# Kernel optimization log

Measured on AMD Instinct MI355X. Metric: run time of the kernel, lower is better.

## Reference

```python
import jax, jax.numpy as jnp
import numpy as np

L = 5        # n_layers
H = 8        # heads
DH = 32      # dim_head = n_hidden // heads
D = 256      # n_hidden
KR = 4       # key_ratio
QKD = KR * DH  # 128, q/k feature dim
IN = 3       # fun_dim + space_dim
OUT = 1      # out_dim
N = 32768    # number of mesh points
EPS = 1e-5

def _ln(x, g, b):
    m = jnp.mean(x, axis=-1, keepdims=True)
    v = jnp.var(x, axis=-1, keepdims=True)
    return (x - m) * jax.lax.rsqrt(v + EPS) * g + b

def _gelu(x):
    return jax.nn.gelu(x, approximate=False)  # torch nn.GELU default (erf)

def setup_inputs() -> dict:
    key = jax.random.key(0)
    ks = iter(jax.random.split(key, 64))
    def w(*s):
        return jax.random.normal(next(ks), s, jnp.float32) * 0.02
    return {
        "x": jax.random.normal(next(ks), (N, IN), jnp.float32),
        # preprocess MLP: Linear(IN,2D)+GELU, Linear(2D,D)
        "pre_w1": w(IN, 2 * D), "pre_b1": jnp.zeros((2 * D,), jnp.float32),
        "pre_w2": w(2 * D, D), "pre_b2": jnp.zeros((D,), jnp.float32),
        "placeholder": jax.random.uniform(next(ks), (D,), jnp.float32) / D,
        # per-block params stacked over L
        "ln1_g": jnp.ones((L, D), jnp.float32), "ln1_b": jnp.zeros((L, D), jnp.float32),
        "inp_w": w(L, D, D), "inp_b": jnp.zeros((L, D), jnp.float32),
        "temp_q": jnp.full((L, H), 0.5, jnp.float32), "temp_k": jnp.full((L, H), 0.5, jnp.float32),
        "wq": w(L, DH, QKD), "wk": w(L, DH, QKD), "wv": w(L, DH, DH),
        "out_w1": w(L, D, D), "out_b1": jnp.zeros((L, D), jnp.float32),
        "out_w2": w(L, D, D), "out_b2": jnp.zeros((L, D), jnp.float32),
        "ln2_g": jnp.ones((L, D), jnp.float32), "ln2_b": jnp.zeros((L, D), jnp.float32),
        "mlp_w1": w(L, D, D), "mlp_b1": jnp.zeros((L, D), jnp.float32),  # mlp_ratio=1 -> hidden=D
        "mlp_w2": w(L, D, D), "mlp_b2": jnp.zeros((L, D), jnp.float32),
        # last-layer head
        "ln3_g": jnp.ones((D,), jnp.float32), "ln3_b": jnp.zeros((D,), jnp.float32),
        "head_w": w(D, OUT), "head_b": jnp.zeros((OUT,), jnp.float32),
    }

def reference(x, pre_w1, pre_b1, pre_w2, pre_b2, placeholder,
              ln1_g, ln1_b, inp_w, inp_b, temp_q, temp_k, wq, wk, wv,
              out_w1, out_b1, out_w2, out_b2, ln2_g, ln2_b,
              mlp_w1, mlp_b1, mlp_w2, mlp_b2, ln3_g, ln3_b, head_w, head_b):
    # preprocess + placeholder bias
    fx = _gelu(x[None] @ pre_w1 + pre_b1) @ pre_w2 + pre_b2  # [1, N, D]
    fx = fx + placeholder
    for i in range(L):
        # --- LinearNO attention block ---
        h = _ln(fx, ln1_g[i], ln1_b[i])
        xm = h @ inp_w[i] + inp_b[i]                       # [1, N, D]
        xm = xm.reshape(1, N, H, DH).transpose(0, 2, 1, 3)  # [1, H, N, DH]
        q = jnp.einsum('bhnd,de->bhne', xm, wq[i])          # [1, H, N, QKD]
        k = jnp.einsum('bhnd,de->bhne', xm, wk[i])          # [1, H, N, QKD]
        v = jnp.einsum('bhnd,dc->bhnc', xm, wv[i])          # [1, H, N, DH]
        tq = jnp.clip(temp_q[i], 0.1, 2.0)[None, :, None, None]
        tk = jnp.clip(temp_k[i], 0.1, 2.0)[None, :, None, None]
        q = jax.nn.softmax(q / tq, axis=-1)  # over feature dim
        k = jax.nn.softmax(k / tk, axis=-2)  # over point dim
        kv = jnp.einsum('bhnd,bhnc->bhdc', k, v)    # [1, H, QKD, DH]
        qkv = jnp.einsum('bhnd,bhdc->bhnc', q, kv)  # [1, H, N, DH]
        qkv = qkv.transpose(0, 2, 1, 3).reshape(1, N, D)
        attn = _gelu(qkv @ out_w1[i] + out_b1[i]) @ out_w2[i] + out_b2[i]
        fx = attn + fx
        # --- MLP block (n_layers=0, res=False: pre + post only) ---
        h2 = _ln(fx, ln2_g[i], ln2_b[i])
        fx = _gelu(h2 @ mlp_w1[i] + mlp_b1[i]) @ mlp_w2[i] + mlp_b2[i] + fx
    # last block head: mlp2(ln_3(fx))
    out = _ln(fx, ln3_g, ln3_b) @ head_w + head_b  # [1, N, OUT]
    return out[0]  # module returns fx[0]
```

## Files before the change

### kernel.cpp

```cpp
#include <hip/hip_runtime.h>
#include <hip/hip_bf16.h>
#include <math.h>

constexpr int NP  = 32768;
constexpr int HH  = 8;

typedef short bf16x8 __attribute__((ext_vector_type(8)));
typedef float f32x4  __attribute__((ext_vector_type(4)));

__device__ __forceinline__ float gelu_f(float x) {
    return 0.5f * x * (1.0f + erff(x * 0.70710678118654752f));
}

__device__ __forceinline__ unsigned short f2bf(float x) {
    union { float f; unsigned u; } v; v.f = x;
    unsigned r = v.u + 0x7fffu + ((v.u >> 16) & 1u);
    return (unsigned short)(r >> 16);
}

__device__ __forceinline__ float bf2f(unsigned short h) {
    union { unsigned u; float f; } v; v.u = ((unsigned)h) << 16;
    return v.f;
}

__global__ __launch_bounds__(256) void transpose_bf16_k(
    const float* __restrict__ src, unsigned short* __restrict__ dst, int K)
{
    __shared__ float tile[32][33];
    int g = blockIdx.z;
    int k0 = blockIdx.x * 32, c0 = blockIdx.y * 32;
    int tx = threadIdx.x & 31, ty = threadIdx.x >> 5;
    const float* s = src + (size_t)g * K * 256;
    unsigned short* d = dst + (size_t)g * 256 * K;
    #pragma unroll
    for (int rr = 0; rr < 4; ++rr) {
        int r = ty + rr * 8;
        tile[r][tx] = s[(size_t)(k0 + r) * 256 + c0 + tx];
    }
    __syncthreads();
    #pragma unroll
    for (int rr = 0; rr < 4; ++rr) {
        int r = ty + rr * 8;
        d[(size_t)(c0 + r) * K + k0 + tx] = f2bf(tile[tx][r]);
    }
}

__global__ __launch_bounds__(256) void transpose_scale_bf16_k(
    const float* __restrict__ src, const float* __restrict__ g,
    unsigned short* __restrict__ dst, int K)
{
    __shared__ float tile[32][33];
    int z = blockIdx.z;
    int k0 = blockIdx.x * 32, c0 = blockIdx.y * 32;
    int tx = threadIdx.x & 31, ty = threadIdx.x >> 5;
    const float* s = src + (size_t)z * K * 256;
    unsigned short* d = dst + (size_t)z * 256 * K;
    #pragma unroll
    for (int rr = 0; rr < 4; ++rr) {
        int r = ty + rr * 8;
        tile[r][tx] = s[(size_t)(k0 + r) * 256 + c0 + tx];
    }
    __syncthreads();
    float gs = g[z * 256 + k0 + tx];
    #pragma unroll
    for (int rr = 0; rr < 4; ++rr) {
        int r = ty + rr * 8;
        d[(size_t)(c0 + r) * K + k0 + tx] = f2bf(gs * tile[tx][r]);
    }
}

__global__ __launch_bounds__(256) void colsum_k(
    const float* __restrict__ W, const float* __restrict__ g,
    const float* __restrict__ b, float* __restrict__ c2, float* __restrict__ c1)
{
    int z = blockIdx.z, c = threadIdx.x;
    const float* Wz = W + (size_t)z * 65536;
    const float* gz = g + z * 256;
    const float* bz = b + z * 256;
    float s2 = 0.f, s1 = 0.f;
    for (int k = 0; k < 256; ++k) {
        float w = Wz[k * 256 + c];
        s2 += gz[k] * w;
        s1 += bz[k] * w;
    }
    c2[z * 256 + c] = s2;
    c1[z * 256 + c] = s1;
}

__global__ __launch_bounds__(256) void prep_wkvT(
    const float* __restrict__ wk, const float* __restrict__ wv,
    const float* __restrict__ wq,
    unsigned short* __restrict__ wkT, unsigned short* __restrict__ wvT,
    unsigned short* __restrict__ wqT)
{
    int l = blockIdx.x, tid = threadIdx.x;
    for (int idx = tid; idx < 4096; idx += 256) {
        int d = idx >> 5, k = idx & 31;
        wkT[l * 4096 + idx] = f2bf(wk[l * 4096 + k * 128 + d]);
        wqT[l * 4096 + idx] = f2bf(wq[l * 4096 + k * 128 + d]);
    }
    for (int idx = tid; idx < 1024; idx += 256) {
        int c = idx >> 5, k = idx & 31;
        wvT[l * 1024 + idx] = f2bf(wv[l * 1024 + k * 32 + c]);
    }
}

template<bool GENA, bool AF32, bool LNFOLD, bool DOGELU, bool RESID, bool STATS, bool PERM>
__global__ __launch_bounds__(256) void gemm_bf(
    const unsigned short* __restrict__ Ah, const float* __restrict__ Af,
    const unsigned short* __restrict__ Wt,
    const float* __restrict__ bias, const float* __restrict__ bias2,
    float* __restrict__ outF, unsigned short* __restrict__ outH,
    const float* __restrict__ stats_in, float* __restrict__ stats_out,
    const float* __restrict__ c1v, const float* __restrict__ c2vec,
    const float* __restrict__ genx, const float* __restrict__ genw1,
    const float* __restrict__ genb1, int K)
{
    __shared__ __align__(16) unsigned short As[128 * 64];
    __shared__ __align__(16) unsigned short Bs[128 * 64];
    __shared__ float rmean[LNFOLD ? 128 : 1];
    __shared__ float rrstd[LNFOLD ? 128 : 1];
    __shared__ float w1s[GENA ? 1536 : 1];
    __shared__ float b1s[GENA ? 512 : 1];
    __shared__ float x3s[GENA ? 512 : 1];

    const int tid = threadIdx.x;
    const int rBase = blockIdx.x * 128, cBase = blockIdx.y * 128;

    if constexpr (GENA) {
        for (int i2 = tid; i2 < 1536; i2 += 256) w1s[i2] = genw1[i2];
        for (int i2 = tid; i2 < 512; i2 += 256) b1s[i2] = genb1[i2];
        if (tid < 128) {
            x3s[tid * 4 + 0] = genx[(size_t)(rBase + tid) * 3 + 0];
            x3s[tid * 4 + 1] = genx[(size_t)(rBase + tid) * 3 + 1];
            x3s[tid * 4 + 2] = genx[(size_t)(rBase + tid) * 3 + 2];
        }
        __syncthreads();
    }
    if constexpr (LNFOLD) {
        if (tid < 128) {
            const float* sp = stats_in + (size_t)(rBase + tid) * 8;
            float4 s0 = *(const float4*)sp;
            float4 s1 = *(const float4*)(sp + 4);
            float mean = (s0.x + s0.z + s1.x + s1.z) * (1.f / 256.f);
            float ex2  = (s0.y + s0.w + s1.y + s1.w) * (1.f / 256.f);
            rmean[tid] = mean;
            rrstd[tid] = rsqrtf(fmaxf(ex2 - mean * mean, 0.f) + 1e-5f);
        }
        __syncthreads();
    }

    f32x4 acc[4][4];
    #pragma unroll
    for (int i = 0; i < 4; ++i)
        #pragma unroll
        for (int j = 0; j < 4; ++j)
            acc[i][j] = (f32x4){0.f, 0.f, 0.f, 0.f};

    const int lane = tid & 63, wid = tid >> 6;
    const int wr = wid >> 1, wc = wid & 1;
    const int lrow = lane & 15, quad = lane >> 4;
    const int srow = tid >> 3;
    const int sch  = tid & 7;

    for (int kc = 0; kc < K; kc += 64) {
        if constexpr (GENA) {
            #pragma unroll
            for (int it = 0; it < 4; ++it) {
                int row = srow + it * 32;
                float x0 = x3s[row * 4 + 0], x1 = x3s[row * 4 + 1], x2 = x3s[row * 4 + 2];
                unsigned short pk[8];
                #pragma unroll
                for (int j = 0; j < 8; ++j) {
                    int k = kc + sch * 8 + j;
                    float t = x0 * w1s[k] + x1 * w1s[512 + k] + x2 * w1s[1024 + k] + b1s[k];
                    pk[j] = f2bf(gelu_f(t));
                }
                *(uint4*)&As[row * 64 + ((sch ^ (row & 7)) << 3)] = *(uint4*)pk;
            }
        } else if constexpr (AF32) {
            #pragma unroll
            for (int it = 0; it < 4; ++it) {
                int row = srow + it * 32;
                const float* ap = Af + (size_t)(rBase + row) * K + kc + sch * 8;
                float4 a0 = *(const float4*)ap;
                float4 a1 = *(const float4*)(ap + 4);
                unsigned short pk[8];
                pk[0] = f2bf(a0.x); pk[1] = f2bf(a0.y); pk[2] = f2bf(a0.z); pk[3] = f2bf(a0.w);
                pk[4] = f2bf(a1.x); pk[5] = f2bf(a1.y); pk[6] = f2bf(a1.z); pk[7] = f2bf(a1.w);
                *(uint4*)&As[row * 64 + ((sch ^ (row & 7)) << 3)] = *(uint4*)pk;
            }
        } else {
            #pragma unroll
            for (int it = 0; it < 4; ++it) {
                int row = srow + it * 32;
                uint4 av = *(const uint4*)(Ah + (size_t)(rBase + row) * K + kc + sch * 8);
                *(uint4*)&As[row * 64 + ((sch ^ (row & 7)) << 3)] = av;
            }
        }
        #pragma unroll
        for (int it = 0; it < 4; ++it) {
            int n = srow + it * 32;
            uint4 wv_ = *(const uint4*)(Wt + (size_t)(cBase + n) * K + kc + sch * 8);
            *(uint4*)&Bs[n * 64 + ((sch ^ (n & 7)) << 3)] = wv_;
        }
        __syncthreads();
        #pragma unroll
        for (int ks = 0; ks < 2; ++ks) {
            bf16x8 af[4], bfr[4];
            #pragma unroll
            for (int t = 0; t < 4; ++t) {
                int row = wr * 64 + t * 16 + lrow;
                af[t] = *(bf16x8*)&As[row * 64 + (((ks * 4 + quad) ^ (row & 7)) << 3)];
                int n = wc * 64 + t * 16 + lrow;
                bfr[t] = *(bf16x8*)&Bs[n * 64 + (((ks * 4 + quad) ^ (n & 7)) << 3)];
            }
            #pragma unroll
            for (int ti = 0; ti < 4; ++ti)
                #pragma unroll
                for (int tj = 0; tj < 4; ++tj)
                    acc[ti][tj] = __builtin_amdgcn_mfma_f32_16x16x32_bf16(
                        af[ti], bfr[tj], acc[ti][tj], 0, 0, 0);
        }
        __syncthreads();
    }

    float c1b[4], c2r[4];
    #pragma unroll
    for (int tj = 0; tj < 4; ++tj) {
        int gcol = cBase + wc * 64 + tj * 16 + lrow;
        float b = bias[gcol];
        if (bias2) b += bias2[gcol];
        if constexpr (LNFOLD) {
            c1b[tj] = c1v[gcol] + b;
            c2r[tj] = c2vec[gcol];
        } else {
            c1b[tj] = b;
            c2r[tj] = 0.f;
        }
    }
    #pragma unroll
    for (int ti = 0; ti < 4; ++ti) {
        #pragma unroll
        for (int r = 0; r < 4; ++r) {
            int rib = wr * 64 + ti * 16 + quad * 4 + r;
            int grow = rBase + rib;
            float mean = 0.f, rstd = 1.f;
            if constexpr (LNFOLD) { mean = rmean[rib]; rstd = rrstd[rib]; }
            float vv[4];
            #pragma unroll
            for (int tj = 0; tj < 4; ++tj) {
                float t = acc[ti][tj][r];
                float v;
                if constexpr (LNFOLD) v = rstd * (t - mean * c2r[tj]) + c1b[tj];
                else                  v = t + c1b[tj];
                if constexpr (DOGELU) v = gelu_f(v);
                vv[tj] = v;
            }
            if constexpr (RESID) {
                #pragma unroll
                for (int tj = 0; tj < 4; ++tj) {
                    int gcol = cBase + wc * 64 + tj * 16 + lrow;
                    vv[tj] += outF[(size_t)grow * 256 + gcol];
                }
            }
            if constexpr (STATS) {
                float rs = vv[0] + vv[1] + vv[2] + vv[3];
                float rq = vv[0]*vv[0] + vv[1]*vv[1] + vv[2]*vv[2] + vv[3]*vv[3];
                #pragma unroll
                for (int m = 1; m < 16; m <<= 1) {
                    rs += __shfl_xor(rs, m);
                    rq += __shfl_xor(rq, m);
                }
                if (lrow == 0) {
                    stats_out[(size_t)grow * 8 + (blockIdx.y * 2 + wc) * 2 + 0] = rs;
                    stats_out[(size_t)grow * 8 + (blockIdx.y * 2 + wc) * 2 + 1] = rq;
                }
            }
            #pragma unroll
            for (int tj = 0; tj < 4; ++tj) {
                int gcol = cBase + wc * 64 + tj * 16 + lrow;
                if constexpr (PERM) {
                    size_t pidx = (size_t)(gcol >> 5) * NP * 32 + (size_t)grow * 32 + (gcol & 31);
                    if (outF) outF[pidx] = vv[tj];
                    if (outH) outH[pidx] = f2bf(vv[tj]);
                } else {
                    if (outF) outF[(size_t)grow * 256 + gcol] = vv[tj];
                    if (outH) outH[(size_t)grow * 256 + gcol] = f2bf(vv[tj]);
                }
            }
        }
    }
}

template<bool AF32, bool LNFOLD>
__global__ __launch_bounds__(256) void gemm_lgl(
    const unsigned short* __restrict__ Ah, const float* __restrict__ Af,
    const unsigned short* __restrict__ W1t, const unsigned short* __restrict__ W2t,
    const float* __restrict__ b1, const float* __restrict__ b2,
    float* __restrict__ fx,
    const float* __restrict__ stats_in, float* __restrict__ stats_out,
    const float* __restrict__ c1v, const float* __restrict__ c2vec)
{
    __shared__ __align__(16) unsigned short As[64 * 64];
    __shared__ __align__(16) unsigned short Bs[256 * 64];
    __shared__ __align__(16) unsigned short Ts[64 * 256];
    __shared__ float rmean[LNFOLD ? 64 : 1];
    __shared__ float rrstd[LNFOLD ? 64 : 1];

    const int tid = threadIdx.x;
    const int rBase = blockIdx.x * 64;
    const int lane = tid & 63, wid = tid >> 6;
    const int lrow = lane & 15, quad = lane >> 4;

    if constexpr (LNFOLD) {
        if (tid < 64) {
            const float* sp = stats_in + (size_t)(rBase + tid) * 8;
            float4 s0 = *(const float4*)sp;
            float4 s1 = *(const float4*)(sp + 4);
            float mean = (s0.x + s0.z + s1.x + s1.z) * (1.f / 256.f);
            float ex2  = (s0.y + s0.w + s1.y + s1.w) * (1.f / 256.f);
            rmean[tid] = mean;
            rrstd[tid] = rsqrtf(fmaxf(ex2 - mean * mean, 0.f) + 1e-5f);
        }
    }

    f32x4 acc[4][4];
    #pragma unroll
    for (int i = 0; i < 4; ++i)
        #pragma unroll
        for (int j = 0; j < 4; ++j)
            acc[i][j] = (f32x4){0.f, 0.f, 0.f, 0.f};

    for (int kc = 0; kc < 256; kc += 64) {
        #pragma unroll
        for (int it = 0; it < 2; ++it) {
            int idx = tid + it * 256;
            int row = idx >> 3, sch = idx & 7;
            if constexpr (AF32) {
                const float* ap = Af + (size_t)(rBase + row) * 256 + kc + sch * 8;
                float4 a0 = *(const float4*)ap;
                float4 a1 = *(const float4*)(ap + 4);
                unsigned short pk[8];
                pk[0] = f2bf(a0.x); pk[1] = f2bf(a0.y); pk[2] = f2bf(a0.z); pk[3] = f2bf(a0.w);
                pk[4] = f2bf(a1.x); pk[5] = f2bf(a1.y); pk[6] = f2bf(a1.z); pk[7] = f2bf(a1.w);
                *(uint4*)&As[row * 64 + ((sch ^ (row & 7)) << 3)] = *(uint4*)pk;
            } else {
                uint4 av = *(const uint4*)(Ah + (size_t)(rBase + row) * 256 + kc + sch * 8);
                *(uint4*)&As[row * 64 + ((sch ^ (row & 7)) << 3)] = av;
            }
        }
        #pragma unroll
        for (int it = 0; it < 8; ++it) {
            int idx = tid + it * 256;
            int n = idx >> 3, sch = idx & 7;
            uint4 wv_ = *(const uint4*)(W1t + (size_t)n * 256 + kc + sch * 8);
            *(uint4*)&Bs[n * 64 + ((sch ^ (n & 7)) << 3)] = wv_;
        }
        __syncthreads();
        #pragma unroll
        for (int ks = 0; ks < 2; ++ks) {
            bf16x8 af[4], bfr[4];
            #pragma unroll
            for (int t = 0; t < 4; ++t) {
                int row = t * 16 + lrow;
                af[t] = *(bf16x8*)&As[row * 64 + (((ks * 4 + quad) ^ (row & 7)) << 3)];
                int n = wid * 64 + t * 16 + lrow;
                bfr[t] = *(bf16x8*)&Bs[n * 64 + (((ks * 4 + quad) ^ (n & 7)) << 3)];
            }
            #pragma unroll
            for (int ti = 0; ti < 4; ++ti)
                #pragma unroll
                for (int tj = 0; tj < 4; ++tj)
                    acc[ti][tj] = __builtin_amdgcn_mfma_f32_16x16x32_bf16(
                        af[ti], bfr[tj], acc[ti][tj], 0, 0, 0);
        }
        __syncthreads();
    }

    {
        float c1b[4], c2r[4];
        #pragma unroll
        for (int tj = 0; tj < 4; ++tj) {
            int gcol = wid * 64 + tj * 16 + lrow;
            if constexpr (LNFOLD) {
                c1b[tj] = c1v[gcol] + b1[gcol];
                c2r[tj] = c2vec[gcol];
            } else {
                c1b[tj] = b1[gcol];
                c2r[tj] = 0.f;
            }
        }
        #pragma unroll
        for (int ti = 0; ti < 4; ++ti) {
            #pragma unroll
            for (int r = 0; r < 4; ++r) {
                int row = ti * 16 + quad * 4 + r;
                float mean = 0.f, rstd = 1.f;
                if constexpr (LNFOLD) { mean = rmean[row]; rstd = rrstd[row]; }
                #pragma unroll
                for (int tj = 0; tj < 4; ++tj) {
                    float t = acc[ti][tj][r];
                    float v;
                    if constexpr (LNFOLD) v = rstd * (t - mean * c2r[tj]) + c1b[tj];
                    else                  v = t + c1b[tj];
                    v = gelu_f(v);
                    int col = wid * 64 + tj * 16 + lrow;
                    int ch = col >> 3;
                    Ts[row * 256 + ((ch ^ (row & 7)) << 3) + (col & 7)] = f2bf(v);
                }
            }
        }
    }
    __syncthreads();

    f32x4 acc2[4][4];
    #pragma unroll
    for (int i = 0; i < 4; ++i)
        #pragma unroll
        for (int j = 0; j < 4; ++j)
            acc2[i][j] = (f32x4){0.f, 0.f, 0.f, 0.f};

    for (int kc = 0; kc < 256; kc += 64) {
        #pragma unroll
        for (int it = 0; it < 8; ++it) {
            int idx = tid + it * 256;
            int n = idx >> 3, sch = idx & 7;
            uint4 wv_ = *(const uint4*)(W2t + (size_t)n * 256 + kc + sch * 8);
            *(uint4*)&Bs[n * 64 + ((sch ^ (n & 7)) << 3)] = wv_;
        }
        __syncthreads();
        #pragma unroll
        for (int ks = 0; ks < 2; ++ks) {
            bf16x8 af[4], bfr[4];
            #pragma unroll
            for (int t = 0; t < 4; ++t) {
                int row = t * 16 + lrow;
                int ch = (kc >> 3) + ks * 4 + quad;
                af[t] = *(bf16x8*)&Ts[row * 256 + ((ch ^ (row & 7)) << 3)];
                int n = wid * 64 + t * 16 + lrow;
                bfr[t] = *(bf16x8*)&Bs[n * 64 + (((ks * 4 + quad) ^ (n & 7)) << 3)];
            }
            #pragma unroll
            for (int ti = 0; ti < 4; ++ti)
                #pragma unroll
                for (int tj = 0; tj < 4; ++tj)
                    acc2[ti][tj] = __builtin_amdgcn_mfma_f32_16x16x32_bf16(
                        af[ti], bfr[tj], acc2[ti][tj], 0, 0, 0);
        }
        __syncthreads();
    }

    float bb[4];
    #pragma unroll
    for (int tj = 0; tj < 4; ++tj) bb[tj] = b2[wid * 64 + tj * 16 + lrow];
    #pragma unroll
    for (int ti = 0; ti < 4; ++ti) {
        #pragma unroll
        for (int r = 0; r < 4; ++r) {
            int grow = rBase + ti * 16 + quad * 4 + r;
            float vv[4];
            #pragma unroll
            for (int tj = 0; tj < 4; ++tj) {
                int gcol = wid * 64 + tj * 16 + lrow;
                vv[tj] = acc2[ti][tj][r] + bb[tj] + fx[(size_t)grow * 256 + gcol];
            }
            float rs = vv[0] + vv[1] + vv[2] + vv[3];
            float rq = vv[0]*vv[0] + vv[1]*vv[1] + vv[2]*vv[2] + vv[3]*vv[3];
            #pragma unroll
            for (int m = 1; m < 16; m <<= 1) {
                rs += __shfl_xor(rs, m);
                rq += __shfl_xor(rq, m);
            }
            if (lrow == 0) {
                stats_out[(size_t)grow * 8 + wid * 2 + 0] = rs;
                stats_out[(size_t)grow * 8 + wid * 2 + 1] = rq;
            }
            #pragma unroll
            for (int tj = 0; tj < 4; ++tj) {
                int gcol = wid * 64 + tj * 16 + lrow;
                fx[(size_t)grow * 256 + gcol] = vv[tj];
            }
        }
    }
}

__global__ __launch_bounds__(256) void kv6_kernel(
    const unsigned short* __restrict__ xm2h, const unsigned short* __restrict__ wkT,
    const unsigned short* __restrict__ wvT, const float* __restrict__ tk_arr,
    float* __restrict__ partials, int layer)
{
    __shared__ __align__(16) unsigned short xs[64 * 32];
    __shared__ __align__(16) unsigned short wks[128 * 32];
    __shared__ __align__(16) unsigned short wvs[32 * 32];
    __shared__ __align__(16) unsigned short els[128 * 72];
    __shared__ __align__(16) unsigned short vls[32 * 72];
    __shared__ float sums[4 * 128];

    const int tid = threadIdx.x;
    const int h = blockIdx.y;
    const int rowBase = blockIdx.x * 512;
    const int w = tid >> 6, lane = tid & 63;
    const int lrow = lane & 15, quad = lane >> 4;

    float tk = fminf(fmaxf(tk_arr[layer * 8 + h], 0.1f), 2.0f);
    float invtk = 1.0f / tk;

    #pragma unroll
    for (int it = 0; it < 2; ++it) {
        int cid = tid + it * 256;
        int d = cid >> 2, kc = cid & 3;
        uint4 v = *(const uint4*)(wkT + d * 32 + kc * 8);
        *(uint4*)&wks[d * 32 + ((kc ^ (d & 3)) << 3)] = v;
    }
    if (tid < 128) {
        int c = tid >> 2, kc = tid & 3;
        uint4 v = *(const uint4*)(wvT + c * 32 + kc * 8);
        *(uint4*)&wvs[c * 32 + ((kc ^ (c & 3)) << 3)] = v;
    }

    f32x4 acc2[2][2];
    #pragma unroll
    for (int di = 0; di < 2; ++di)
        #pragma unroll
        for (int ci = 0; ci < 2; ++ci)
            acc2[di][ci] = (f32x4){0.f, 0.f, 0.f, 0.f};
    float seacc[8];
    #pragma unroll
    for (int dt = 0; dt < 8; ++dt) seacc[dt] = 0.f;

    const unsigned short* src = xm2h + (size_t)h * NP * 32 + (size_t)rowBase * 32;

    for (int sub = 0; sub < 8; ++sub) {
        __syncthreads();
        {
            int row = tid >> 2, kc = tid & 3;
            uint4 v = *(const uint4*)(src + (size_t)(sub * 64 + row) * 32 + kc * 8);
            *(uint4*)&xs[row * 32 + ((kc ^ (row & 3)) << 3)] = v;
        }
        __syncthreads();
        int arow = w * 16 + lrow;
        bf16x8 ax = *(bf16x8*)&xs[arow * 32 + ((quad ^ (arow & 3)) << 3)];
        #pragma unroll
        for (int ct = 0; ct < 2; ++ct) {
            int c = ct * 16 + lrow;
            bf16x8 bw = *(bf16x8*)&wvs[c * 32 + ((quad ^ (c & 3)) << 3)];
            f32x4 cc = (f32x4){0.f, 0.f, 0.f, 0.f};
            cc = __builtin_amdgcn_mfma_f32_16x16x32_bf16(ax, bw, cc, 0, 0, 0);
            unsigned short pk[4];
            pk[0] = f2bf(cc[0]); pk[1] = f2bf(cc[1]);
            pk[2] = f2bf(cc[2]); pk[3] = f2bf(cc[3]);
            *(uint2*)&vls[(ct * 16 + lrow) * 72 + w * 16 + quad * 4] = *(uint2*)pk;
        }
        #pragma unroll
        for (int dt = 0; dt < 8; ++dt) {
            int d = dt * 16 + lrow;
            bf16x8 bw = *(bf16x8*)&wks[d * 32 + ((quad ^ (d & 3)) << 3)];
            f32x4 cc = (f32x4){0.f, 0.f, 0.f, 0.f};
            cc = __builtin_amdgcn_mfma_f32_16x16x32_bf16(ax, bw, cc, 0, 0, 0);
            unsigned short pk[4];
            float se = 0.f;
            #pragma unroll
            for (int r = 0; r < 4; ++r) {
                float l = fminf(fmaxf(cc[r] * invtk, -30.f), 30.f);
                unsigned short eb = f2bf(__expf(l));
                pk[r] = eb;
                se += bf2f(eb);
            }
            seacc[dt] += se;
            *(uint2*)&els[d * 72 + w * 16 + quad * 4] = *(uint2*)pk;
        }
        __syncthreads();
        #pragma unroll
        for (int di = 0; di < 2; ++di) {
            int dm = (2 * w + di) * 16 + lrow;
            #pragma unroll
            for (int ks = 0; ks < 2; ++ks) {
                bf16x8 ae = *(bf16x8*)&els[dm * 72 + ks * 32 + quad * 8];
                #pragma unroll
                for (int ci = 0; ci < 2; ++ci) {
                    int cn = ci * 16 + lrow;
                    bf16x8 bv = *(bf16x8*)&vls[cn * 72 + ks * 32 + quad * 8];
                    acc2[di][ci] = __builtin_amdgcn_mfma_f32_16x16x32_bf16(
                        ae, bv, acc2[di][ci], 0, 0, 0);
                }
            }
        }
    }

    float* outp = partials + ((size_t)h * 64 + blockIdx.x) * 4224;
    #pragma unroll
    for (int di = 0; di < 2; ++di)
        #pragma unroll
        for (int ci = 0; ci < 2; ++ci)
            #pragma unroll
            for (int r = 0; r < 4; ++r) {
                int d = (2 * w + di) * 16 + quad * 4 + r;
                int c = ci * 16 + lrow;
                outp[d * 32 + c] = acc2[di][ci][r];
            }
    #pragma unroll
    for (int dt = 0; dt < 8; ++dt) {
        float s = seacc[dt];
        s += __shfl_xor(s, 16);
        s += __shfl_xor(s, 32);
        if (quad == 0) sums[w * 128 + dt * 16 + lrow] = s;
    }
    __syncthreads();
    if (tid < 128)
        outp[4096 + tid] = sums[tid] + sums[128 + tid] + sums[256 + tid] + sums[384 + tid];
}

__global__ __launch_bounds__(256) void kv_reduce_kernel(
    const float* __restrict__ partials, unsigned short* __restrict__ kvT,
    float* __restrict__ sumexp)
{
    int gid = blockIdx.x * 256 + threadIdx.x;
    if (gid >= 8 * 4224) return;
    int h = gid / 4224, idx = gid % 4224;
    const float* base = partials + (size_t)h * 64 * 4224 + idx;
    float s = 0.f;
    #pragma unroll 8
    for (int c = 0; c < 64; ++c) s += base[(size_t)c * 4224];
    if (idx < 4096) {
        int d = idx >> 5, c = idx & 31;
        kvT[(size_t)h * 4096 + c * 128 + d] = f2bf(s);
    } else {
        sumexp[h * 128 + (idx - 4096)] = s;
    }
}

__global__ __launch_bounds__(256) void qkv6_kernel(
    const unsigned short* __restrict__ xm2h, const unsigned short* __restrict__ wqT,
    const float* __restrict__ tq_arr, const unsigned short* __restrict__ kvT,
    const float* __restrict__ sumexp, unsigned short* __restrict__ outH, int layer)
{
    __shared__ __align__(16) unsigned short xs[64 * 32];
    __shared__ __align__(16) unsigned short wqs[128 * 32];
    __shared__ __align__(16) unsigned short kvb[32 * 136];
    __shared__ __align__(16) unsigned short els[64 * 136];
    __shared__ float ises[128];

    const int tid = threadIdx.x;
    const int h = blockIdx.y;
    const int rowBase = blockIdx.x * 64;
    const int w = tid >> 6, lane = tid & 63;
    const int lrow = lane & 15, quad = lane >> 4;

    float tq = fminf(fmaxf(tq_arr[layer * 8 + h], 0.1f), 2.0f);
    float invtq = 1.0f / tq;

    if (tid < 128) ises[tid] = 1.0f / sumexp[h * 128 + tid];
    #pragma unroll
    for (int it = 0; it < 2; ++it) {
        int cid = tid + it * 256;
        int d = cid >> 2, kc = cid & 3;
        uint4 v = *(const uint4*)(wqT + d * 32 + kc * 8);
        *(uint4*)&wqs[d * 32 + ((kc ^ (d & 3)) << 3)] = v;
    }
    #pragma unroll
    for (int it = 0; it < 2; ++it) {
        int cid = tid + it * 256;
        int c = cid >> 4, k8 = cid & 15;
        uint4 v = *(const uint4*)(kvT + (size_t)h * 4096 + c * 128 + k8 * 8);
        *(uint4*)&kvb[c * 136 + k8 * 8] = v;
    }
    {
        int row = tid >> 2, kc = tid & 3;
        uint4 v = *(const uint4*)(xm2h + (size_t)h * NP * 32 +
                                  (size_t)(rowBase + row) * 32 + kc * 8);
        *(uint4*)&xs[row * 32 + ((kc ^ (row & 3)) << 3)] = v;
    }
    __syncthreads();

    int arow = w * 16 + lrow;
    bf16x8 ax = *(bf16x8*)&xs[arow * 32 + ((quad ^ (arow & 3)) << 3)];
    f32x4 lg[8];
    #pragma unroll
    for (int dt = 0; dt < 8; ++dt) {
        int d = dt * 16 + lrow;
        bf16x8 bw = *(bf16x8*)&wqs[d * 32 + ((quad ^ (d & 3)) << 3)];
        f32x4 cc = (f32x4){0.f, 0.f, 0.f, 0.f};
        lg[dt] = __builtin_amdgcn_mfma_f32_16x16x32_bf16(ax, bw, cc, 0, 0, 0);
    }
    float isv[8];
    #pragma unroll
    for (int dt = 0; dt < 8; ++dt) isv[dt] = ises[dt * 16 + lrow];

    #pragma unroll
    for (int r = 0; r < 4; ++r) {
        float m = lg[0][r];
        #pragma unroll
        for (int dt = 1; dt < 8; ++dt) m = fmaxf(m, lg[dt][r]);
        m = fmaxf(m, __shfl_xor(m, 1));
        m = fmaxf(m, __shfl_xor(m, 2));
        m = fmaxf(m, __shfl_xor(m, 4));
        m = fmaxf(m, __shfl_xor(m, 8));
        float e[8], s = 0.f;
        #pragma unroll
        for (int dt = 0; dt < 8; ++dt) {
            e[dt] = __expf((lg[dt][r] - m) * invtq);
            s += e[dt];
        }
        s += __shfl_xor(s, 1);
        s += __shfl_xor(s, 2);
        s += __shfl_xor(s, 4);
        s += __shfl_xor(s, 8);
        float inv = 1.0f / s;
        int erow = w * 16 + quad * 4 + r;
        #pragma unroll
        for (int dt = 0; dt < 8; ++dt)
            els[erow * 136 + dt * 16 + lrow] = f2bf(e[dt] * inv * isv[dt]);
    }

    #pragma unroll
    for (int ct = 0; ct < 2; ++ct) {
        f32x4 oc = (f32x4){0.f, 0.f, 0.f, 0.f};
        #pragma unroll
        for (int ks = 0; ks < 4; ++ks) {
            bf16x8 ae = *(bf16x8*)&els[(w * 16 + lrow) * 136 + ks * 32 + quad * 8];
            bf16x8 bv = *(bf16x8*)&kvb[(ct * 16 + lrow) * 136 + ks * 32 + quad * 8];
            oc = __builtin_amdgcn_mfma_f32_16x16x32_bf16(ae, bv, oc, 0, 0, 0);
        }
        #pragma unroll
        for (int r = 0; r < 4; ++r)
            outH[(size_t)(rowBase + w * 16 + quad * 4 + r) * 256 +
                 h * 32 + ct * 16 + lrow] = f2bf(oc[r]);
    }
}

__global__ __launch_bounds__(256) void head_kernel(
    const float* __restrict__ fx, const float* __restrict__ g, const float* __restrict__ b,
    const float* __restrict__ hw, const float* __restrict__ hb, float* __restrict__ out)
{
    int lane = threadIdx.x & 63;
    int row = blockIdx.x * 4 + (threadIdx.x >> 6);
    float4 v = *(const float4*)(fx + (size_t)row * 256 + lane * 4);
    float s1 = v.x + v.y + v.z + v.w;
    float s2 = v.x * v.x + v.y * v.y + v.z * v.z + v.w * v.w;
    #pragma unroll
    for (int m = 1; m < 64; m <<= 1) { s1 += __shfl_xor(s1, m); s2 += __shfl_xor(s2, m); }
    float mean = s1 * 0.00390625f;
    float rstd = rsqrtf(fmaxf(s2 * 0.00390625f - mean * mean, 0.f) + 1e-5f);
    float4 gg = *(const float4*)(g + lane * 4);
    float4 bb = *(const float4*)(b + lane * 4);
    float4 w4 = *(const float4*)(hw + lane * 4);
    float d = ((v.x - mean) * rstd * gg.x + bb.x) * w4.x
            + ((v.y - mean) * rstd * gg.y + bb.y) * w4.y
            + ((v.z - mean) * rstd * gg.z + bb.z) * w4.z
            + ((v.w - mean) * rstd * gg.w + bb.w) * w4.w;
    #pragma unroll
    for (int m = 1; m < 64; m <<= 1) d += __shfl_xor(d, m);
    if (lane == 0) out[row] = d + hb[0];
}

extern "C" void kernel_launch(void* const* d_in, const int* in_sizes, int n_in,
                              void* d_out, int out_size, void* d_ws, size_t ws_size,
                              hipStream_t stream)
{
    const float* x      = (const float*)d_in[0];
    const float* pre_w1 = (const float*)d_in[1];
    const float* pre_b1 = (const float*)d_in[2];
    const float* pre_w2 = (const float*)d_in[3];
    const float* pre_b2 = (const float*)d_in[4];
    const float* ph     = (const float*)d_in[5];
    const float* ln1_g  = (const float*)d_in[6];
    const float* ln1_b  = (const float*)d_in[7];
    const float* inp_w  = (const float*)d_in[8];
    const float* inp_b  = (const float*)d_in[9];
    const float* temp_q = (const float*)d_in[10];
    const float* temp_k = (const float*)d_in[11];
    const float* wq     = (const float*)d_in[12];
    const float* wk     = (const float*)d_in[13];
    const float* wv     = (const float*)d_in[14];
    const float* out_w1 = (const float*)d_in[15];
    const float* out_b1 = (const float*)d_in[16];
    const float* out_w2 = (const float*)d_in[17];
    const float* out_b2 = (const float*)d_in[18];
    const float* ln2_g  = (const float*)d_in[19];
    const float* ln2_b  = (const float*)d_in[20];
    const float* mlp_w1 = (const float*)d_in[21];
    const float* mlp_b1 = (const float*)d_in[22];
    const float* mlp_w2 = (const float*)d_in[23];
    const float* mlp_b2 = (const float*)d_in[24];
    const float* ln3_g  = (const float*)d_in[25];
    const float* ln3_b  = (const float*)d_in[26];
    const float* head_w = (const float*)d_in[27];
    const float* head_b = (const float*)d_in[28];
    float* out = (float*)d_out;

    float* fx = (float*)d_ws;
    unsigned short* fxh = (unsigned short*)(fx + (size_t)NP * 256);
    unsigned short* ChH = fxh + (size_t)NP * 256;
    unsigned short* xm2h = ChH;
    float* scr = (float*)(ChH + (size_t)NP * 256);
    float* st = scr + (size_t)NP * 256;
    unsigned short* kvT = (unsigned short*)(st + (size_t)NP * 8);
    float* se = (float*)(kvT + 8 * 4096);
    float* c1i = se + 8 * 128;
    float* c2i = c1i + 1280;
    float* c1m = c2i + 1280;
    float* c2m = c1m + 1280;
    unsigned short* wtPre = (unsigned short*)(c2m + 1280);
    unsigned short* wtL   = wtPre + 256 * 512;
    unsigned short* wkT   = wtL + 25 * 65536;
    unsigned short* wvT   = wkT + 5 * 4096;
    unsigned short* wqT   = wvT + 5 * 1024;

    unsigned short* wtIn = wtL;
    unsigned short* wtO1 = wtL +  5 * 65536;
    unsigned short* wtO2 = wtL + 10 * 65536;
    unsigned short* wtM1 = wtL + 15 * 65536;
    unsigned short* wtM2 = wtL + 20 * 65536;

    unsigned short* qh = (unsigned short*)scr;

    dim3 bt(256);

    transpose_bf16_k<<<dim3(16, 8, 1), bt, 0, stream>>>(pre_w2, wtPre, 512);
    transpose_scale_bf16_k<<<dim3(8, 8, 5), bt, 0, stream>>>(inp_w,  ln1_g, wtIn, 256);
    transpose_bf16_k<<<dim3(8, 8, 5), bt, 0, stream>>>(out_w1, wtO1, 256);
    transpose_bf16_k<<<dim3(8, 8, 5), bt, 0, stream>>>(out_w2, wtO2, 256);
    transpose_scale_bf16_k<<<dim3(8, 8, 5), bt, 0, stream>>>(mlp_w1, ln2_g, wtM1, 256);
    transpose_bf16_k<<<dim3(8, 8, 5), bt, 0, stream>>>(mlp_w2, wtM2, 256);
    colsum_k<<<dim3(1, 1, 5), bt, 0, stream>>>(inp_w,  ln1_g, ln1_b, c2i, c1i);
    colsum_k<<<dim3(1, 1, 5), bt, 0, stream>>>(mlp_w1, ln2_g, ln2_b, c2m, c1m);
    prep_wkvT<<<dim3(5), bt, 0, stream>>>(wk, wv, wq, wkT, wvT, wqT);

    dim3 gg(256, 2);

    gemm_bf<true, false, false, false, false, true, false><<<gg, bt, 0, stream>>>(
        nullptr, nullptr, wtPre, pre_b2, ph, fx, nullptr, nullptr, st,
        nullptr, nullptr, x, pre_w1, pre_b1, 512);

    for (int i = 0; i < 5; ++i) {
        gemm_bf<false, true, true, false, false, false, true><<<gg, bt, 0, stream>>>(
            nullptr, fx, wtIn + (size_t)i * 65536, inp_b + i * 256, nullptr, nullptr, xm2h,
            st, nullptr, c1i + i * 256, c2i + i * 256, nullptr, nullptr, nullptr, 256);
        kv6_kernel<<<dim3(64, 8), bt, 0, stream>>>(
            xm2h, wkT + (size_t)i * 4096, wvT + (size_t)i * 1024, temp_k, scr, i);
        kv_reduce_kernel<<<dim3(132), bt, 0, stream>>>(scr, kvT, se);
        qkv6_kernel<<<dim3(512, 8), bt, 0, stream>>>(
            xm2h, wqT + (size_t)i * 4096, temp_q, kvT, se, qh, i);
        gemm_lgl<false, false><<<dim3(512), bt, 0, stream>>>(
            qh, nullptr, wtO1 + (size_t)i * 65536, wtO2 + (size_t)i * 65536,
            out_b1 + i * 256, out_b2 + i * 256, fx, nullptr, st, nullptr, nullptr);
        gemm_lgl<true, true><<<dim3(512), bt, 0, stream>>>(
            nullptr, fx, wtM1 + (size_t)i * 65536, wtM2 + (size_t)i * 65536,
            mlp_b1 + i * 256, mlp_b2 + i * 256, fx, st, st,
            c1m + i * 256, c2m + i * 256);
    }
    head_kernel<<<dim3(NP / 4), bt, 0, stream>>>(fx, ln3_g, ln3_b, head_w, head_b, out);
}
```

Before: 830.5 us.

## Fuse next layer's LN1+input projection into MLP gemm epilogue

The MLP gemm_lgl kernel now keeps its output rows in shared memory as bf16. It computes per-row LayerNorm statistics locally and runs the next layer's input-projection GEMM (LN folded via c1/c2 vectors) in the same kernel, writing xm2h directly. This removes one launch per layer and the re-read of fx and stats from global memory. The costs are extra register and LDS pressure in the fused kernel, and the last layer's stats are no longer written.

```diff
diff --git a/kernel.cpp b/kernel.cpp
--- a/kernel.cpp
+++ b/kernel.cpp
@@ -293,20 +293,25 @@
     }
 }
 
-template<bool AF32, bool LNFOLD>
+template<bool AF32, bool LNFOLD, bool WSTATS, bool NEXTW>
 __global__ __launch_bounds__(256) void gemm_lgl(
     const unsigned short* __restrict__ Ah, const float* __restrict__ Af,
     const unsigned short* __restrict__ W1t, const unsigned short* __restrict__ W2t,
     const float* __restrict__ b1, const float* __restrict__ b2,
     float* __restrict__ fx,
     const float* __restrict__ stats_in, float* __restrict__ stats_out,
-    const float* __restrict__ c1v, const float* __restrict__ c2vec)
+    const float* __restrict__ c1v, const float* __restrict__ c2vec,
+    const unsigned short* __restrict__ W3t, const float* __restrict__ b3,
+    const float* __restrict__ c1n, const float* __restrict__ c2n,
+    unsigned short* __restrict__ outNext)
 {
     __shared__ __align__(16) unsigned short As[64 * 64];
     __shared__ __align__(16) unsigned short Bs[256 * 64];
     __shared__ __align__(16) unsigned short Ts[64 * 256];
-    __shared__ float rmean[LNFOLD ? 64 : 1];
-    __shared__ float rrstd[LNFOLD ? 64 : 1];
+    __shared__ float rmean[(LNFOLD || NEXTW) ? 64 : 1];
+    __shared__ float rrstd[(LNFOLD || NEXTW) ? 64 : 1];
+    __shared__ float ssum[NEXTW ? 256 : 1];
+    __shared__ float ssq [NEXTW ? 256 : 1];
 
     const int tid = threadIdx.x;
     const int rBase = blockIdx.x * 64;
@@ -458,28 +463,118 @@
     for (int ti = 0; ti < 4; ++ti) {
         #pragma unroll
         for (int r = 0; r < 4; ++r) {
-            int grow = rBase + ti * 16 + quad * 4 + r;
+            int row = ti * 16 + quad * 4 + r;
+            int grow = rBase + row;
             float vv[4];
             #pragma unroll
             for (int tj = 0; tj < 4; ++tj) {
                 int gcol = wid * 64 + tj * 16 + lrow;
                 vv[tj] = acc2[ti][tj][r] + bb[tj] + fx[(size_t)grow * 256 + gcol];
             }
-            float rs = vv[0] + vv[1] + vv[2] + vv[3];
-            float rq = vv[0]*vv[0] + vv[1]*vv[1] + vv[2]*vv[2] + vv[3]*vv[3];
-            #pragma unroll
-            for (int m = 1; m < 16; m <<= 1) {
-                rs += __shfl_xor(rs, m);
-                rq += __shfl_xor(rq, m);
-            }
-            if (lrow == 0) {
-                stats_out[(size_t)grow * 8 + wid * 2 + 0] = rs;
-                stats_out[(size_t)grow * 8 + wid * 2 + 1] = rq;
+            if constexpr (WSTATS || NEXTW) {
+                float rs = vv[0] + vv[1] + vv[2] + vv[3];
+                float rq = vv[0]*vv[0] + vv[1]*vv[1] + vv[2]*vv[2] + vv[3]*vv[3];
+                #pragma unroll
+                for (int m = 1; m < 16; m <<= 1) {
+                    rs += __shfl_xor(rs, m);
+                    rq += __shfl_xor(rq, m);
+                }
+                if (lrow == 0) {
+                    if constexpr (WSTATS) {
+                        stats_out[(size_t)grow * 8 + wid * 2 + 0] = rs;
+                        stats_out[(size_t)grow * 8 + wid * 2 + 1] = rq;
+                    }
+                    if constexpr (NEXTW) {
+                        ssum[row * 4 + wid] = rs;
+                        ssq [row * 4 + wid] = rq;
+                    }
+                }
             }
             #pragma unroll
             for (int tj = 0; tj < 4; ++tj) {
                 int gcol = wid * 64 + tj * 16 + lrow;
                 fx[(size_t)grow * 256 + gcol] = vv[tj];
+                if constexpr (NEXTW) {
+                    int ch = gcol >> 3;
+                    Ts[row * 256 + ((ch ^ (row & 7)) << 3) + (gcol & 7)] = f2bf(vv[tj]);
+                }
+            }
+        }
+    }
+
+    if constexpr (NEXTW) {
+        __syncthreads();
+        if (tid < 64) {
+            float q0 = ssum[tid * 4 + 0], q1 = ssum[tid * 4 + 1];
+            float q2 = ssum[tid * 4 + 2], q3 = ssum[tid * 4 + 3];
+            float p0 = ssq [tid * 4 + 0], p1 = ssq [tid * 4 + 1];
+            float p2 = ssq [tid * 4 + 2], p3 = ssq [tid * 4 + 3];
+            float mean = (q0 + q1 + q2 + q3) * (1.f / 256.f);
+            float ex2  = (p0 + p1 + p2 + p3) * (1.f / 256.f);
+            rmean[tid] = mean;
+            rrstd[tid] = rsqrtf(fmaxf(ex2 - mean * mean, 0.f) + 1e-5f);
+        }
+        __syncthreads();
+
+        f32x4 acc3[4][4];
+        #pragma unroll
+        for (int i = 0; i < 4; ++i)
+            #pragma unroll
+            for (int j = 0; j < 4; ++j)
+                acc3[i][j] = (f32x4){0.f, 0.f, 0.f, 0.f};
+
+        for (int kc = 0; kc < 256; kc += 64) {
+            #pragma unroll
+            for (int it = 0; it < 8; ++it) {
+                int idx = tid + it * 256;
+                int n = idx >> 3, sch = idx & 7;
+                uint4 wv_ = *(const uint4*)(W3t + (size_t)n * 256 + kc + sch * 8);
+                *(uint4*)&Bs[n * 64 + ((sch ^ (n & 7)) << 3)] = wv_;
+            }
+            __syncthreads();
+            #pragma unroll
+            for (int ks = 0; ks < 2; ++ks) {
+                bf16x8 af[4], bfr[4];
+                #pragma unroll
+                for (int t = 0; t < 4; ++t) {
+                    int row = t * 16 + lrow;
+                    int ch = (kc >> 3) + ks * 4 + quad;
+                    af[t] = *(bf16x8*)&Ts[row * 256 + ((ch ^ (row & 7)) << 3)];
+                    int n = wid * 64 + t * 16 + lrow;
+                    bfr[t] = *(bf16x8*)&Bs[n * 64 + (((ks * 4 + quad) ^ (n & 7)) << 3)];
+                }
+                #pragma unroll
+                for (int ti = 0; ti < 4; ++ti)
+                    #pragma unroll
+                    for (int tj = 0; tj < 4; ++tj)
+                        acc3[ti][tj] = __builtin_amdgcn_mfma_f32_16x16x32_bf16(
+                            af[ti], bfr[tj], acc3[ti][tj], 0, 0, 0);
+            }
+            __syncthreads();
+        }
+
+        float c1b3[4], c2r3[4];
+        #pragma unroll
+        for (int tj = 0; tj < 4; ++tj) {
+            int gcol = wid * 64 + tj * 16 + lrow;
+            c1b3[tj] = c1n[gcol] + b3[gcol];
+            c2r3[tj] = c2n[gcol];
+        }
+        #pragma unroll
+        for (int ti = 0; ti < 4; ++ti) {
+            #pragma unroll
+            for (int r = 0; r < 4; ++r) {
+                int row = ti * 16 + quad * 4 + r;
+                int grow = rBase + row;
+                float mean = rmean[row], rstd = rrstd[row];
+                #pragma unroll
+                for (int tj = 0; tj < 4; ++tj) {
+                    int gcol = wid * 64 + tj * 16 + lrow;
+                    float t = acc3[ti][tj][r];
+                    float v = rstd * (t - mean * c2r3[tj]) + c1b3[tj];
+                    size_t pidx = (size_t)(gcol >> 5) * NP * 32 + (size_t)grow * 32 + (gcol & 31);
+                    outNext[pidx] = f2bf(v);
+                }
             }
         }
     }
@@ -833,22 +928,34 @@
         nullptr, nullptr, wtPre, pre_b2, ph, fx, nullptr, nullptr, st,
         nullptr, nullptr, x, pre_w1, pre_b1, 512);
 
+    gemm_bf<false, true, true, false, false, false, true><<<gg, bt, 0, stream>>>(
+        nullptr, fx, wtIn, inp_b, nullptr, nullptr, xm2h,
+        st, nullptr, c1i, c2i, nullptr, nullptr, nullptr, 256);
+
     for (int i = 0; i < 5; ++i) {
-        gemm_bf<false, true, true, false, false, false, true><<<gg, bt, 0, stream>>>(
-            nullptr, fx, wtIn + (size_t)i * 65536, inp_b + i * 256, nullptr, nullptr, xm2h,
-            st, nullptr, c1i + i * 256, c2i + i * 256, nullptr, nullptr, nullptr, 256);
         kv6_kernel<<<dim3(64, 8), bt, 0, stream>>>(
             xm2h, wkT + (size_t)i * 4096, wvT + (size_t)i * 1024, temp_k, scr, i);
         kv_reduce_kernel<<<dim3(132), bt, 0, stream>>>(scr, kvT, se);
         qkv6_kernel<<<dim3(512, 8), bt, 0, stream>>>(
             xm2h, wqT + (size_t)i * 4096, temp_q, kvT, se, qh, i);
-        gemm_lgl<false, false><<<dim3(512), bt, 0, stream>>>(
+        gemm_lgl<false, false, true, false><<<dim3(512), bt, 0, stream>>>(
             qh, nullptr, wtO1 + (size_t)i * 65536, wtO2 + (size_t)i * 65536,
-            out_b1 + i * 256, out_b2 + i * 256, fx, nullptr, st, nullptr, nullptr);
-        gemm_lgl<true, true><<<dim3(512), bt, 0, stream>>>(
-            nullptr, fx, wtM1 + (size_t)i * 65536, wtM2 + (size_t)i * 65536,
-            mlp_b1 + i * 256, mlp_b2 + i * 256, fx, st, st,
-            c1m + i * 256, c2m + i * 256);
+            out_b1 + i * 256, out_b2 + i * 256, fx, nullptr, st, nullptr, nullptr,
+            nullptr, nullptr, nullptr, nullptr, nullptr);
+        if (i < 4) {
+            gemm_lgl<true, true, false, true><<<dim3(512), bt, 0, stream>>>(
+                nullptr, fx, wtM1 + (size_t)i * 65536, wtM2 + (size_t)i * 65536,
+                mlp_b1 + i * 256, mlp_b2 + i * 256, fx, st, nullptr,
+                c1m + i * 256, c2m + i * 256,
+                wtIn + (size_t)(i + 1) * 65536, inp_b + (i + 1) * 256,
+                c1i + (i + 1) * 256, c2i + (i + 1) * 256, xm2h);
+        } else {
+            gemm_lgl<true, true, false, false><<<dim3(512), bt, 0, stream>>>(
+                nullptr, fx, wtM1 + (size_t)i * 65536, wtM2 + (size_t)i * 65536,
+                mlp_b1 + i * 256, mlp_b2 + i * 256, fx, st, nullptr,
+                c1m + i * 256, c2m + i * 256,
+                nullptr, nullptr, nullptr, nullptr, nullptr);
+        }
     }
     head_kernel<<<dim3(NP / 4), bt, 0, stream>>>(fx, ln3_g, ln3_b, head_w, head_b, out);
 }
```

Measured after the change: 809.4 us. -2.5%, faster.
